# Kernel optimization log

Hardware: AMD Instinct MI355X
Metric: run time of the kernel (lower is better)

## Reference

```python
import jax, jax.numpy as jnp
import numpy as np

N = 50000   # nodes
E = 600000  # edges
D = 128     # in = hidden = out channels
L = 3       # num_layers
LN_EPS = 1e-5


def setup_inputs() -> dict:
    key = jax.random.key(0)
    ks = jax.random.split(key, 4)
    x = jax.random.normal(ks[0], (N, D), dtype=jnp.float32)
    edge_index = jax.random.randint(ks[1], (2, E), 0, N, dtype=jnp.int32)
    # GCNConv linear weights (glorot-ish scale) and biases, one per layer
    Ws = jax.random.normal(ks[2], (L, D, D), dtype=jnp.float32) / np.sqrt(D)
    bs = jnp.zeros((L, D), dtype=jnp.float32)
    # LayerNorm affine params per layer
    ln_w = jnp.ones((L, D), dtype=jnp.float32)
    ln_b = jnp.zeros((L, D), dtype=jnp.float32)
    # PReLU (single shared slope per layer, torch default init 0.25)
    alphas = jnp.full((L,), 0.25, dtype=jnp.float32)
    return {"x": x, "edge_index": edge_index, "Ws": Ws, "bs": bs,
            "ln_w": ln_w, "ln_b": ln_b, "alphas": alphas}


def reference(x, edge_index, Ws, bs, ln_w, ln_b, alphas):
    # --- gcn_norm: add self-loops, symmetric D^{-1/2} (A+I) D^{-1/2} ---
    loop = jnp.arange(N, dtype=edge_index.dtype)
    src = jnp.concatenate([edge_index[0], loop])  # [E+N]
    dst = jnp.concatenate([edge_index[1], loop])  # [E+N]
    deg = jax.ops.segment_sum(jnp.ones_like(dst, dtype=x.dtype), dst,
                              num_segments=N)
    dinv = jnp.where(deg > 0, jax.lax.rsqrt(jnp.maximum(deg, 1.0)), 0.0)
    norm = (dinv[src] * dinv[dst])[:, None]  # [E+N, 1]

    h = x
    for l in range(L):
        # GCNConv: linear -> gather -> scale -> scatter-add -> bias
        h = h @ Ws[l]                                   # [N, D]
        msg = h[src] * norm                             # [E+N, D]
        h = jax.ops.segment_sum(msg, dst, num_segments=N) + bs[l]
        # LayerNorm over feature dim
        mu = jnp.mean(h, axis=-1, keepdims=True)
        var = jnp.mean((h - mu) ** 2, axis=-1, keepdims=True)
        h = (h - mu) * jax.lax.rsqrt(var + LN_EPS) * ln_w[l] + ln_b[l]
        # PReLU
        h = jnp.where(h >= 0, h, alphas[l] * h)
    return h
```

## Files before the change

### kernel.cpp

```cpp
#include <hip/hip_runtime.h>
#include <hip/hip_bf16.h>

#define NN 50000
#define EE 600000
#define DD 128
#define LL 3
#define LN_EPS 1e-5f
#define CAP 64
#define ALD 136
#define POOL 128

typedef __attribute__((ext_vector_type(8))) short short8;
typedef __attribute__((ext_vector_type(4))) float floatx4;

__device__ inline unsigned short f2bf(float f) {
    union { float f; unsigned u; } a; a.f = f;
    unsigned r = a.u + 0x7fffu + ((a.u >> 16) & 1u);
    return (unsigned short)(r >> 16);
}


__global__ void fill_kernel(const int* __restrict__ src, const int* __restrict__ dst,
                            const float* __restrict__ W, unsigned short* __restrict__ Wt,
                            int* __restrict__ cnt, int* __restrict__ csrc) {
    int i = blockIdx.x * blockDim.x + threadIdx.x;
    if (i < LL * DD * DD) {
        int l = i >> 14, n = (i >> 7) & 127, k = i & 127;
        Wt[i] = f2bf(W[(l << 14) + k * DD + n]);
    }
    if (i >= EE) return;
    int d = dst[i];
    int pos = atomicAdd(&cnt[d], 1);
    csrc[(size_t)d * CAP + pos] = src[i];
}


__global__ __launch_bounds__(256) void gemm0_kernel(const float* __restrict__ A,
                                                    const unsigned short* __restrict__ Wt,
                                                    const int* __restrict__ cnt,
                                                    unsigned short* __restrict__ Cb) {
    __shared__ unsigned short alds[32 * ALD];
    int tid = threadIdx.x;
    int lane = tid & 63;
    int w = tid >> 6;
    int rowbase = blockIdx.x * 32;

    int cbase = (w & 1) * 64;
    int nIdx = cbase + (lane & 15);
    int kq = (lane >> 4) * 8;

    {
        int r = tid >> 3;
        int k0 = (tid & 7) * 16;
        int grow = rowbase + r;
        unsigned short* dstp = &alds[r * ALD + k0];
        if (grow < NN) {
            const float* ap = &A[(size_t)grow * DD + k0];
            float4 v0 = *(const float4*)&ap[0];
            float4 v1 = *(const float4*)&ap[4];
            float4 v2 = *(const float4*)&ap[8];
            float4 v3 = *(const float4*)&ap[12];
            float fv[16] = {v0.x,v0.y,v0.z,v0.w, v1.x,v1.y,v1.z,v1.w,
                            v2.x,v2.y,v2.z,v2.w, v3.x,v3.y,v3.z,v3.w};
            unsigned short uv[16];
            #pragma unroll
            for (int q = 0; q < 16; q++) uv[q] = f2bf(fv[q]);
            *(uint4*)&dstp[0] = *(uint4*)&uv[0];
            *(uint4*)&dstp[8] = *(uint4*)&uv[8];
        } else {
            uint4 z = make_uint4(0, 0, 0, 0);
            *(uint4*)&dstp[0] = z;
            *(uint4*)&dstp[8] = z;
        }
    }
    __syncthreads();

    int rbase = (w >> 1) * 16;
    int mrow = rbase + (lane & 15);
    floatx4 acc[4] = {{0.f,0.f,0.f,0.f},{0.f,0.f,0.f,0.f},
                      {0.f,0.f,0.f,0.f},{0.f,0.f,0.f,0.f}};
    #pragma unroll
    for (int t = 0; t < 4; t++) {
        short8 a = *(const short8*)&alds[mrow * ALD + t * 32 + kq];
        #pragma unroll
        for (int j = 0; j < 4; j++) {
            short8 b = *(const short8*)&Wt[(nIdx + j * 16) * DD + t * 32 + kq];
            acc[j] = __builtin_amdgcn_mfma_f32_16x16x32_bf16(a, b, acc[j], 0, 0, 0);
        }
    }

    int gnode0 = rowbase + rbase + (lane >> 4) * 4;
    #pragma unroll
    for (int i = 0; i < 4; i++) {
        int node = gnode0 + i;
        if (node < NN) {
            float dv = rsqrtf((float)(cnt[node] + 1));
            #pragma unroll
            for (int j = 0; j < 4; j++)
                Cb[(size_t)node * DD + cbase + j * 16 + (lane & 15)] = f2bf(acc[j][i] * dv);
        }
    }
}


__device__ inline void acc_row(float* acc, uint4 t) {
    unsigned uu[4] = {t.x, t.y, t.z, t.w};
    #pragma unroll
    for (int q = 0; q < 4; q++) {
        union { unsigned x; float f; } lo, hi;
        lo.x = uu[q] << 16;
        hi.x = uu[q] & 0xffff0000u;
        acc[2 * q]     += lo.f;
        acc[2 * q + 1] += hi.f;
    }
}

__device__ inline void agg_node(const unsigned short* __restrict__ Tb,
                                const int* __restrict__ cnt, const int* __restrict__ csrc,
                                const float* bv, const float* wv, const float* cv,
                                float alpha, int node, int f8, float* yv) {
    int deg = cnt[node];
    float dv = rsqrtf((float)(deg + 1));
    const int* row = &csrc[(size_t)node * CAP];

    float acc[8] = {};
    acc_row(acc, *(const uint4*)&Tb[(size_t)node * DD + f8]);

    int k = 0;
    for (; k + 4 <= deg; k += 4) {
        int4 ss = *(const int4*)&row[k];
        uint4 t0 = *(const uint4*)&Tb[(size_t)ss.x * DD + f8];
        uint4 t1 = *(const uint4*)&Tb[(size_t)ss.y * DD + f8];
        uint4 t2 = *(const uint4*)&Tb[(size_t)ss.z * DD + f8];
        uint4 t3 = *(const uint4*)&Tb[(size_t)ss.w * DD + f8];
        acc_row(acc, t0); acc_row(acc, t1); acc_row(acc, t2); acc_row(acc, t3);
    }
    for (; k < deg; k++) {
        acc_row(acc, *(const uint4*)&Tb[(size_t)row[k] * DD + f8]);
    }

    float a[8];
    float s1 = 0.f, s2 = 0.f;
    #pragma unroll
    for (int q = 0; q < 8; q++) {
        a[q] = fmaf(acc[q], dv, bv[q]);
        s1 += a[q]; s2 += a[q] * a[q];
    }
    #pragma unroll
    for (int off = 8; off > 0; off >>= 1) {
        s1 += __shfl_xor(s1, off, 16);
        s2 += __shfl_xor(s2, off, 16);
    }
    float mu = s1 * (1.f / DD);
    float var = s2 * (1.f / DD) - mu * mu;
    float rstd = rsqrtf(var + LN_EPS);
    #pragma unroll
    for (int q = 0; q < 8; q++) {
        float y = (a[q] - mu) * rstd * wv[q] + cv[q];
        yv[q] = (y >= 0.f) ? y : alpha * y;
    }
}


__global__ __launch_bounds__(512) void aggemm_kernel(
    const unsigned short* __restrict__ Tb, const int* __restrict__ cnt,
    const int* __restrict__ csrc,
    const float* __restrict__ bias, const float* __restrict__ lnw,
    const float* __restrict__ lnb, const float* __restrict__ alphas, int layer,
    const unsigned short* __restrict__ Wt, unsigned short* __restrict__ Tout) {
    __shared__ unsigned short alds[POOL * ALD];
    __shared__ int nextslot;
    int tid = threadIdx.x;
    int lane16 = tid & 15;
    int f8 = lane16 * 8;
    int nodebase = blockIdx.x * POOL;
    if (tid == 0) nextslot = 0;

    float4 b0 = *(const float4*)&bias[f8];
    float4 b1 = *(const float4*)&bias[f8 + 4];
    float4 w0 = *(const float4*)&lnw[f8];
    float4 w1 = *(const float4*)&lnw[f8 + 4];
    float4 c0 = *(const float4*)&lnb[f8];
    float4 c1 = *(const float4*)&lnb[f8 + 4];
    float bv[8] = {b0.x, b0.y, b0.z, b0.w, b1.x, b1.y, b1.z, b1.w};
    float wv[8] = {w0.x, w0.y, w0.z, w0.w, w1.x, w1.y, w1.z, w1.w};
    float cv[8] = {c0.x, c0.y, c0.z, c0.w, c1.x, c1.y, c1.z, c1.w};
    float alpha = alphas[layer];
    __syncthreads();

    for (;;) {
        int sv = 0;
        if (lane16 == 0) sv = atomicAdd(&nextslot, 1);
        int s = __shfl(sv, 0, 16);
        if (s >= POOL) break;
        int node = nodebase + s;
        unsigned short* dstp = &alds[s * ALD + f8];
        if (node < NN) {
            float yv[8];
            agg_node(Tb, cnt, csrc, bv, wv, cv, alpha, node, f8, yv);
            unsigned short pv[8];
            #pragma unroll
            for (int q = 0; q < 8; q++) pv[q] = f2bf(yv[q]);
            *(uint4*)dstp = *(uint4*)&pv[0];
        } else {
            *(uint4*)dstp = make_uint4(0, 0, 0, 0);
        }
    }
    __syncthreads();

    int lane = tid & 63;
    int w = tid >> 6;
    int rbase = w * 16;
    int kq = (lane >> 4) * 8;
    int mrow = rbase + (lane & 15);
    int nIdx = lane & 15;
    floatx4 acc[8] = {{0.f,0.f,0.f,0.f},{0.f,0.f,0.f,0.f},{0.f,0.f,0.f,0.f},
                      {0.f,0.f,0.f,0.f},{0.f,0.f,0.f,0.f},{0.f,0.f,0.f,0.f},
                      {0.f,0.f,0.f,0.f},{0.f,0.f,0.f,0.f}};
    #pragma unroll
    for (int t = 0; t < 4; t++) {
        short8 a = *(const short8*)&alds[mrow * ALD + t * 32 + kq];
        #pragma unroll
        for (int j = 0; j < 8; j++) {
            short8 b = *(const short8*)&Wt[(nIdx + j * 16) * DD + t * 32 + kq];
            acc[j] = __builtin_amdgcn_mfma_f32_16x16x32_bf16(a, b, acc[j], 0, 0, 0);
        }
    }
    int gnode0 = nodebase + rbase + (lane >> 4) * 4;
    #pragma unroll
    for (int i = 0; i < 4; i++) {
        int node = gnode0 + i;
        if (node < NN) {
            float dv = rsqrtf((float)(cnt[node] + 1));
            #pragma unroll
            for (int j = 0; j < 8; j++)
                Tout[(size_t)node * DD + j * 16 + (lane & 15)] = f2bf(acc[j][i] * dv);
        }
    }
}


__global__ __launch_bounds__(256) void agg_final_kernel(
    const unsigned short* __restrict__ Tb, const int* __restrict__ cnt,
    const int* __restrict__ csrc,
    const float* __restrict__ bias, const float* __restrict__ lnw,
    const float* __restrict__ lnb, const float* __restrict__ alphas, int layer,
    float* __restrict__ out) {
    int g = threadIdx.x >> 4;
    int lane16 = threadIdx.x & 15;
    int f8 = lane16 * 8;
    int node = blockIdx.x * 16 + g;
    if (node >= NN) return;

    float4 b0 = *(const float4*)&bias[f8];
    float4 b1 = *(const float4*)&bias[f8 + 4];
    float4 w0 = *(const float4*)&lnw[f8];
    float4 w1 = *(const float4*)&lnw[f8 + 4];
    float4 c0 = *(const float4*)&lnb[f8];
    float4 c1 = *(const float4*)&lnb[f8 + 4];
    float bv[8] = {b0.x, b0.y, b0.z, b0.w, b1.x, b1.y, b1.z, b1.w};
    float wv[8] = {w0.x, w0.y, w0.z, w0.w, w1.x, w1.y, w1.z, w1.w};
    float cv[8] = {c0.x, c0.y, c0.z, c0.w, c1.x, c1.y, c1.z, c1.w};

    float yv[8];
    agg_node(Tb, cnt, csrc, bv, wv, cv, alphas[layer], node, f8, yv);

    float* op = &out[(size_t)node * DD + f8];
    *(float4*)&op[0] = make_float4(yv[0], yv[1], yv[2], yv[3]);
    *(float4*)&op[4] = make_float4(yv[4], yv[5], yv[6], yv[7]);
}


extern "C" void kernel_launch(void* const* d_in, const int* in_sizes, int n_in,
                              void* d_out, int out_size, void* d_ws, size_t ws_size,
                              hipStream_t stream) {
    const float* x    = (const float*)d_in[0];
    const int*   ei   = (const int*)d_in[1];
    const float* Ws   = (const float*)d_in[2];
    const float* bs   = (const float*)d_in[3];
    const float* lnw  = (const float*)d_in[4];
    const float* lnb  = (const float*)d_in[5];
    const float* alphas = (const float*)d_in[6];
    float* out = (float*)d_out;

    const int* src = ei;
    const int* dst = ei + EE;

    char* ws = (char*)d_ws;
    size_t off = 0;
    auto alloc = [&](size_t bytes) -> void* {
        void* p = ws + off;
        off = (off + bytes + 255) & ~(size_t)255;
        return p;
    };
    int* cnt  = (int*)alloc(NN * sizeof(int));
    int* csrc = (int*)alloc((size_t)NN * CAP * sizeof(int));
    unsigned short* wt    = (unsigned short*)alloc((size_t)LL * DD * DD * sizeof(unsigned short));
    unsigned short* tbufA = (unsigned short*)alloc((size_t)NN * DD * sizeof(unsigned short));
    unsigned short* tbufB = (unsigned short*)alloc((size_t)NN * DD * sizeof(unsigned short));

    hipMemsetAsync(cnt, 0, NN * sizeof(int), stream);
    fill_kernel<<<(EE + 255) / 256, 256, 0, stream>>>(src, dst, Ws, wt, cnt, csrc);

    gemm0_kernel<<<(NN + 31) / 32, 256, 0, stream>>>(x, wt, cnt, tbufA);

    const int agg_grid = (NN + POOL - 1) / POOL;
    aggemm_kernel<<<agg_grid, 512, 0, stream>>>(tbufA, cnt, csrc,
                                                bs + 0 * DD, lnw + 0 * DD, lnb + 0 * DD,
                                                alphas, 0, wt + 1 * DD * DD, tbufB);
    aggemm_kernel<<<agg_grid, 512, 0, stream>>>(tbufB, cnt, csrc,
                                                bs + 1 * DD, lnw + 1 * DD, lnb + 1 * DD,
                                                alphas, 1, wt + 2 * DD * DD, tbufA);
    agg_final_kernel<<<(NN + 15) / 16, 256, 0, stream>>>(tbufA, cnt, csrc,
                                                         bs + 2 * DD, lnw + 2 * DD, lnb + 2 * DD,
                                                         alphas, 2, out);
}
```

Measured before the change: 254.7 us.

## Shrink aggregate-GEMM blocks to 16 nodes with static assignment and column-split MFMA

Each aggemm block now handles 16 nodes with 256 threads instead of 128 nodes with 512 threads. It drops the shared-memory atomic work queue, so each 16-lane group aggregates one fixed node. The GEMM now splits the 128 output columns across 4 waves instead of splitting rows. The aim is many more, smaller blocks for better load balance and occupancy, with no atomics. The cost is that each block re-reads the whole W tile for only 16 rows, and the bounds checks are removed because NN divides evenly by 16.

Measured after the change: 243.6 us. -4.4%, faster.

```diff
diff --git a/kernel.cpp b/kernel.cpp
--- a/kernel.cpp
+++ b/kernel.cpp
@@ -8,7 +8,7 @@
 #define LN_EPS 1e-5f
 #define CAP 64
 #define ALD 136
-#define POOL 128
+#define POOL 16
 
 typedef __attribute__((ext_vector_type(8))) short short8;
 typedef __attribute__((ext_vector_type(4))) float floatx4;
@@ -162,19 +162,18 @@
 }
 
 
-__global__ __launch_bounds__(512) void aggemm_kernel(
+__global__ __launch_bounds__(256) void aggemm_kernel(
     const unsigned short* __restrict__ Tb, const int* __restrict__ cnt,
     const int* __restrict__ csrc,
     const float* __restrict__ bias, const float* __restrict__ lnw,
     const float* __restrict__ lnb, const float* __restrict__ alphas, int layer,
     const unsigned short* __restrict__ Wt, unsigned short* __restrict__ Tout) {
     __shared__ unsigned short alds[POOL * ALD];
-    __shared__ int nextslot;
     int tid = threadIdx.x;
+    int g = tid >> 4;
     int lane16 = tid & 15;
     int f8 = lane16 * 8;
     int nodebase = blockIdx.x * POOL;
-    if (tid == 0) nextslot = 0;
 
     float4 b0 = *(const float4*)&bias[f8];
     float4 b1 = *(const float4*)&bias[f8 + 4];
@@ -186,56 +185,41 @@
     float wv[8] = {w0.x, w0.y, w0.z, w0.w, w1.x, w1.y, w1.z, w1.w};
     float cv[8] = {c0.x, c0.y, c0.z, c0.w, c1.x, c1.y, c1.z, c1.w};
     float alpha = alphas[layer];
-    __syncthreads();
-
-    for (;;) {
-        int sv = 0;
-        if (lane16 == 0) sv = atomicAdd(&nextslot, 1);
-        int s = __shfl(sv, 0, 16);
-        if (s >= POOL) break;
-        int node = nodebase + s;
-        unsigned short* dstp = &alds[s * ALD + f8];
-        if (node < NN) {
-            float yv[8];
-            agg_node(Tb, cnt, csrc, bv, wv, cv, alpha, node, f8, yv);
-            unsigned short pv[8];
-            #pragma unroll
-            for (int q = 0; q < 8; q++) pv[q] = f2bf(yv[q]);
-            *(uint4*)dstp = *(uint4*)&pv[0];
-        } else {
-            *(uint4*)dstp = make_uint4(0, 0, 0, 0);
-        }
+
+    {
+        int node = nodebase + g;
+        float yv[8];
+        agg_node(Tb, cnt, csrc, bv, wv, cv, alpha, node, f8, yv);
+        unsigned short pv[8];
+        #pragma unroll
+        for (int q = 0; q < 8; q++) pv[q] = f2bf(yv[q]);
+        *(uint4*)&alds[g * ALD + f8] = *(uint4*)&pv[0];
     }
     __syncthreads();
 
     int lane = tid & 63;
     int w = tid >> 6;
-    int rbase = w * 16;
+    int cbase = w * 32;
     int kq = (lane >> 4) * 8;
-    int mrow = rbase + (lane & 15);
-    int nIdx = lane & 15;
-    floatx4 acc[8] = {{0.f,0.f,0.f,0.f},{0.f,0.f,0.f,0.f},{0.f,0.f,0.f,0.f},
-                      {0.f,0.f,0.f,0.f},{0.f,0.f,0.f,0.f},{0.f,0.f,0.f,0.f},
-                      {0.f,0.f,0.f,0.f},{0.f,0.f,0.f,0.f}};
+    int mrow = lane & 15;
+    floatx4 acc[2] = {{0.f,0.f,0.f,0.f},{0.f,0.f,0.f,0.f}};
     #pragma unroll
     for (int t = 0; t < 4; t++) {
         short8 a = *(const short8*)&alds[mrow * ALD + t * 32 + kq];
         #pragma unroll
-        for (int j = 0; j < 8; j++) {
-            short8 b = *(const short8*)&Wt[(nIdx + j * 16) * DD + t * 32 + kq];
+        for (int j = 0; j < 2; j++) {
+            short8 b = *(const short8*)&Wt[(cbase + j * 16 + (lane & 15)) * DD + t * 32 + kq];
             acc[j] = __builtin_amdgcn_mfma_f32_16x16x32_bf16(a, b, acc[j], 0, 0, 0);
         }
     }
-    int gnode0 = nodebase + rbase + (lane >> 4) * 4;
+    int gnode0 = nodebase + (lane >> 4) * 4;
     #pragma unroll
     for (int i = 0; i < 4; i++) {
         int node = gnode0 + i;
-        if (node < NN) {
-            float dv = rsqrtf((float)(cnt[node] + 1));
-            #pragma unroll
-            for (int j = 0; j < 8; j++)
-                Tout[(size_t)node * DD + j * 16 + (lane & 15)] = f2bf(acc[j][i] * dv);
-        }
+        float dv = rsqrtf((float)(cnt[node] + 1));
+        #pragma unroll
+        for (int j = 0; j < 2; j++)
+            Tout[(size_t)node * DD + cbase + j * 16 + (lane & 15)] = f2bf(acc[j][i] * dv);
     }
 }
 
@@ -304,11 +288,11 @@
 
     gemm0_kernel<<<(NN + 31) / 32, 256, 0, stream>>>(x, wt, cnt, tbufA);
 
-    const int agg_grid = (NN + POOL - 1) / POOL;
-    aggemm_kernel<<<agg_grid, 512, 0, stream>>>(tbufA, cnt, csrc,
+    const int agg_grid = NN / POOL;
+    aggemm_kernel<<<agg_grid, 256, 0, stream>>>(tbufA, cnt, csrc,
                                                 bs + 0 * DD, lnw + 0 * DD, lnb + 0 * DD,
                                                 alphas, 0, wt + 1 * DD * DD, tbufB);
-    aggemm_kernel<<<agg_grid, 512, 0, stream>>>(tbufB, cnt, csrc,
+    aggemm_kernel<<<agg_grid, 256, 0, stream>>>(tbufB, cnt, csrc,
                                                 bs + 1 * DD, lnw + 1 * DD, lnb + 1 * DD,
                                                 alphas, 1, wt + 2 * DD * DD, tbufA);
     agg_final_kernel<<<(NN + 15) / 16, 256, 0, stream>>>(tbufA, cnt, csrc,
```
